# Kernel optimization log

Hardware: AMD Instinct MI355X
Metric: run time of the kernel (lower is better)

The kernel has to match this reference:

```python
import jax, jax.numpy as jnp
import numpy as np

NUM_HEADS = 8


def setup_inputs() -> dict:
    key = jax.random.key(0)
    ks = jax.random.split(key, 6)
    B, E, L = 8, 256, 4096
    top_k = 256
    return {
        "query": jax.random.normal(ks[0], (B, E, L), jnp.float32),
        "keys": jax.random.normal(ks[1], (B, E, L), jnp.float32),
        "values": jax.random.normal(ks[2], (B, E, L), jnp.float32),
        "rand_token_ind": jax.random.randint(ks[3], (B, top_k), 0, L),
        "in_proj_weight": jax.random.normal(ks[4], (3 * E, E), jnp.float32) / np.float32(np.sqrt(E)),
        "in_proj_bias": jnp.zeros((3 * E,), jnp.float32),
        "out_proj_weight": jax.random.normal(ks[5], (E, E), jnp.float32) / np.float32(np.sqrt(E)),
        "out_proj_bias": jnp.zeros((E,), jnp.float32),
        "top_k": top_k,
    }


def _forward(query, keys, values, rand_token_ind, in_proj_weight, in_proj_bias,
             out_proj_weight, out_proj_bias, top_k):
    B, E, Lq = query.shape
    # flatten(2).transpose(-1,-2): channel-first -> [B, L, E]
    q = jnp.swapaxes(query, 1, 2)
    k = jnp.swapaxes(keys, 1, 2)
    v = jnp.swapaxes(values, 1, 2)

    # --- dist_to_random_Q_selection ---
    # random subset of queries, [B, S, E]
    Q_small = jnp.take_along_axis(q, rand_token_ind[:, :, None], axis=1)

    # running min over subset queries of L1 distance (avoids [B,Lk,S,D] blowup)
    def step(min_d, qs):  # qs: [B, E]
        d = jnp.sum(jnp.abs(k - qs[:, None, :]), axis=-1)  # [B, Lk]
        return jnp.minimum(min_d, d), None

    init = jnp.full((B, k.shape[1]), jnp.inf, dtype=k.dtype)
    min_d, _ = jax.lax.scan(step, init, jnp.swapaxes(Q_small, 0, 1))

    # top_k smallest distances, sorted ascending (torch largest=False, sorted=True)
    _, idx = jax.lax.top_k(-min_d, top_k)  # idx: [B, top_k]
    sk = jnp.take_along_axis(k, idx[:, :, None], axis=1)  # [B, top_k, E]
    sv = jnp.take_along_axis(v, idx[:, :, None], axis=1)

    # --- standard torch MultiheadAttention (batch_first) ---
    Wq, Wk, Wv = jnp.split(in_proj_weight, 3, axis=0)
    bq, bk, bv = jnp.split(in_proj_bias, 3, axis=0)
    hd = E // NUM_HEADS
    scale = hd ** -0.5

    def heads(x):
        return x.reshape(x.shape[0], x.shape[1], NUM_HEADS, hd)

    qh = heads(q @ Wq.T + bq) * scale      # [B, Lq, H, hd]
    kh = heads(sk @ Wk.T + bk)             # [B, K,  H, hd]
    vh = heads(sv @ Wv.T + bv)

    scores = jnp.einsum('bqhd,bkhd->bhqk', qh, kh)
    attn = jax.nn.softmax(scores, axis=-1)
    o = jnp.einsum('bhqk,bkhd->bqhd', attn, vh).reshape(B, Lq, E)
    out = o @ out_proj_weight.T + out_proj_bias  # [B, Lq, E]

    # transpose back to original [B, E, Lq] layout
    return jnp.swapaxes(out, 1, 2)


def reference(query, keys, values, rand_token_ind, in_proj_weight, in_proj_bias,
              out_proj_weight, out_proj_bias, top_k):
    return _forward(query, keys, values, rand_token_ind, in_proj_weight,
                    in_proj_bias, out_proj_weight, out_proj_bias, top_k)
```

## Files before the change

kernel.cpp:

```cpp
#include <hip/hip_runtime.h>
#include <math.h>

#define B_SZ   8
#define E_DIM  256
#define L_SEQ  4096
#define S_TOP  256
#define NHEAD  8
#define HD     32
#define NSPLIT 4
#define JSPL   8

typedef __attribute__((ext_vector_type(8))) short bf16x8;
typedef __attribute__((ext_vector_type(4))) float f32x4;

__device__ inline short f2bf(float x) {
    union { float f; unsigned u; } v; v.f = x;
    unsigned r = (v.u + 0x7fff + ((v.u >> 16) & 1)) >> 16;
    return (short)r;
}
__device__ inline float bf2f(short h) {
    union { unsigned u; float f; } c; c.u = ((unsigned)(unsigned short)h) << 16;
    return c.f;
}

__global__ __launch_bounds__(256) void k_gather(const float* __restrict__ query,
                                                const int* __restrict__ ind,
                                                float* __restrict__ qs_pack) {
    int t = blockIdx.x * 256 + threadIdx.x;
    int e = t & (E_DIM - 1);
    int s = (t >> 8) & (S_TOP - 1);
    int b = t >> 16;
    int idx = ind[b * S_TOP + s];
    qs_pack[t] = query[((size_t)b * E_DIM + e) * L_SEQ + idx];
}

__global__ __launch_bounds__(256) void k_dist(const float* __restrict__ keys,
                                              const float* __restrict__ qs_pack,
                                              double* __restrict__ minpart) {
    const int b  = blockIdx.z;
    const int ss = blockIdx.y;
    const int l0 = blockIdx.x * 64;
    const int lid = threadIdx.x;
    const int tx = lid & 15;
    const int ty = lid >> 4;
    __shared__ float Ks[32][64];
    __shared__ float Qs[64][36];
    double (*red)[64] = (double(*)[64])&Ks[0][0];

    const float* kb = keys + (size_t)b * E_DIM * L_SEQ + l0;
    const float* qb = qs_pack + ((size_t)b * S_TOP + ss * 64) * E_DIM;

    double d[4][4];
#pragma unroll
    for (int i = 0; i < 4; ++i)
#pragma unroll
        for (int j = 0; j < 4; ++j) d[i][j] = 0.0;

    for (int c0 = 0; c0 < E_DIM; c0 += 32) {
        __syncthreads();
#pragma unroll
        for (int r = 0; r < 2; ++r) {
            int f4 = lid + 256 * r;
            int e  = f4 >> 4, l4 = (f4 & 15) * 4;
            *(float4*)&Ks[e][l4] = *(const float4*)(kb + (size_t)(c0 + e) * L_SEQ + l4);
            int s  = f4 >> 3, e4 = (f4 & 7) * 4;
            *(float4*)&Qs[s][e4] = *(const float4*)(qb + (size_t)s * E_DIM + c0 + e4);
        }
        __syncthreads();

        float cs[4][4] = {};
#pragma unroll
        for (int e4 = 0; e4 < 32; e4 += 4) {
            float qv[4][4];
#pragma unroll
            for (int j = 0; j < 4; ++j) {
                float4 q = *(const float4*)&Qs[ty * 4 + j][e4];
                qv[j][0] = q.x; qv[j][1] = q.y; qv[j][2] = q.z; qv[j][3] = q.w;
            }
#pragma unroll
            for (int ee = 0; ee < 4; ++ee) {
                float kv[4];
#pragma unroll
                for (int i = 0; i < 4; ++i) kv[i] = Ks[e4 + ee][tx * 4 + i];
#pragma unroll
                for (int i = 0; i < 4; ++i)
#pragma unroll
                    for (int j = 0; j < 4; ++j)
                        cs[i][j] += fabsf(kv[i] - qv[j][ee]);
            }
        }
#pragma unroll
        for (int i = 0; i < 4; ++i)
#pragma unroll
            for (int j = 0; j < 4; ++j) d[i][j] += (double)cs[i][j];
    }

    double md[4];
#pragma unroll
    for (int i = 0; i < 4; ++i) {
        double m = d[i][0];
        m = fmin(m, d[i][1]);
        m = fmin(m, d[i][2]);
        m = fmin(m, d[i][3]);
        md[i] = m;
    }
    __syncthreads();
#pragma unroll
    for (int i = 0; i < 4; ++i) red[ty][tx * 4 + i] = md[i];
    __syncthreads();
    if (lid < 64) {
        double m = red[0][lid];
#pragma unroll
        for (int t = 1; t < 16; ++t) m = fmin(m, red[t][lid]);
        minpart[((size_t)(b * NSPLIT + ss)) * L_SEQ + l0 + lid] = m;
    }
}

__global__ __launch_bounds__(256) void k_rankpart(const double* __restrict__ minpart,
                                                  int* __restrict__ rankpart) {
    const int b  = blockIdx.z;
    const int js = blockIdx.y;
    const int l  = blockIdx.x * 256 + threadIdx.x;
    __shared__ double sd[512];
    const double* mp = minpart + (size_t)b * NSPLIT * L_SEQ;
    for (int jj = threadIdx.x; jj < 512; jj += 256) {
        const int j = js * 512 + jj;
        double v = mp[j];
        v = fmin(v, mp[L_SEQ + j]);
        v = fmin(v, mp[2 * L_SEQ + j]);
        v = fmin(v, mp[3 * L_SEQ + j]);
        sd[jj] = v;
    }
    double dl = mp[l];
    dl = fmin(dl, mp[L_SEQ + l]);
    dl = fmin(dl, mp[2 * L_SEQ + l]);
    dl = fmin(dl, mp[3 * L_SEQ + l]);
    __syncthreads();
    const int jbase = js * 512;
    int rank = 0;
#pragma unroll 8
    for (int jj = 0; jj < 512; ++jj) {
        double dj = sd[jj];
        rank += (dj < dl) || (dj == dl && (jbase + jj) < l) ? 1 : 0;
    }
    rankpart[((size_t)(b * JSPL + js)) * L_SEQ + l] = rank;
}

__global__ __launch_bounds__(256) void k_sel(const int* __restrict__ rankpart,
                                             int* __restrict__ sel) {
    const int t = blockIdx.x * 256 + threadIdx.x;
    const int b = t >> 12;
    const int l = t & (L_SEQ - 1);
    int r = 0;
#pragma unroll
    for (int s = 0; s < JSPL; ++s)
        r += rankpart[((size_t)(b * JSPL + s)) * L_SEQ + l];
    if (r < S_TOP) sel[b * S_TOP + r] = l;
}

__global__ __launch_bounds__(256) void k_kvproj2(const float* __restrict__ keys,
                                                 const float* __restrict__ vals,
                                                 const int* __restrict__ sel,
                                                 const float* __restrict__ Wk,
                                                 const float* __restrict__ bk,
                                                 const float* __restrict__ Wv,
                                                 const float* __restrict__ bv,
                                                 short* __restrict__ khb,
                                                 short* __restrict__ vtb) {
    const int b  = blockIdx.z;
    const int f0 = blockIdx.x * 64;
    const int TR = blockIdx.y >> 2;
    const int k0 = (blockIdx.y & 3) * 64;
    const float* src  = TR ? vals : keys;
    const float* W    = TR ? Wv : Wk;
    const float* bias = TR ? bv : bk;
    const int tx = threadIdx.x, ty = threadIdx.y;
    const int lid = ty * 16 + tx;
    __shared__ float As[16][68];
    __shared__ float Ws[16][68];
    float c[4][4] = {};
    const float* sb = src + (size_t)b * E_DIM * L_SEQ;
    const int* selb = sel + b * S_TOP;
    for (int e0 = 0; e0 < E_DIM; e0 += 16) {
        {
            int e  = lid >> 4;
            int k4 = (lid & 15) * 4;
#pragma unroll
            for (int c2 = 0; c2 < 4; ++c2) {
                int kk = k4 + c2;
                As[e][kk] = sb[(size_t)(e0 + e) * L_SEQ + selb[k0 + kk]];
            }
        }
        {
            int f  = lid >> 2;
            int e4 = (lid & 3) * 4;
            float4 w = *(const float4*)(W + (size_t)(f0 + f) * E_DIM + e0 + e4);
            Ws[e4 + 0][f] = w.x; Ws[e4 + 1][f] = w.y;
            Ws[e4 + 2][f] = w.z; Ws[e4 + 3][f] = w.w;
        }
        __syncthreads();
#pragma unroll
        for (int e = 0; e < 16; ++e) {
            float4 a = *(const float4*)&As[e][ty * 4];
            float4 w = *(const float4*)&Ws[e][tx * 4];
            float av[4] = {a.x, a.y, a.z, a.w};
            float wv[4] = {w.x, w.y, w.z, w.w};
#pragma unroll
            for (int i = 0; i < 4; ++i)
#pragma unroll
                for (int j = 0; j < 4; ++j) c[i][j] += av[i] * wv[j];
        }
        __syncthreads();
    }
    if (TR == 0) {
#pragma unroll
        for (int i = 0; i < 4; ++i) {
            short4 o;
            o.x = f2bf(c[i][0] + bias[f0 + tx * 4 + 0]);
            o.y = f2bf(c[i][1] + bias[f0 + tx * 4 + 1]);
            o.z = f2bf(c[i][2] + bias[f0 + tx * 4 + 2]);
            o.w = f2bf(c[i][3] + bias[f0 + tx * 4 + 3]);
            *(short4*)(khb + ((size_t)b * S_TOP + k0 + ty * 4 + i) * E_DIM + f0 + tx * 4) = o;
        }
    } else {
#pragma unroll
        for (int j = 0; j < 4; ++j) {
            const float bvv = bias[f0 + tx * 4 + j];
            short4 o;
            o.x = f2bf(c[0][j] + bvv); o.y = f2bf(c[1][j] + bvv);
            o.z = f2bf(c[2][j] + bvv); o.w = f2bf(c[3][j] + bvv);
            *(short4*)(vtb + ((size_t)b * E_DIM + f0 + tx * 4 + j) * S_TOP + k0 + ty * 4) = o;
        }
    }
}

__global__ __launch_bounds__(256) void k_wconv(const float* __restrict__ wq,
                                               const float* __restrict__ wo,
                                               short* __restrict__ wqhi,
                                               short* __restrict__ wqlo,
                                               short* __restrict__ wohi,
                                               short* __restrict__ wolo) {
    int t = blockIdx.x * 256 + threadIdx.x;
    float xq = wq[t];
    short hq = f2bf(xq);
    wqhi[t] = hq;
    wqlo[t] = f2bf(xq - bf2f(hq));
    float xo = wo[t];
    short ho = f2bf(xo);
    wohi[t] = ho;
    wolo[t] = f2bf(xo - bf2f(ho));
}

__global__ __launch_bounds__(256) void k_qconv(const float* __restrict__ query,
                                               short* __restrict__ qhi,
                                               short* __restrict__ qlo) {
    const int b  = blockIdx.z;
    const int e0 = blockIdx.y * 64;
    const int l0 = blockIdx.x * 64;
    __shared__ float T[64][68];
    const float* src = query + ((size_t)b * E_DIM + e0) * L_SEQ + l0;
#pragma unroll
    for (int r = 0; r < 4; ++r) {
        int idx = threadIdx.x + 256 * r;
        int e = idx >> 4, l4 = (idx & 15) * 4;
        *(float4*)&T[e][l4] = *(const float4*)(src + (size_t)e * L_SEQ + l4);
    }
    __syncthreads();
    const int l  = threadIdx.x >> 2;
    const int ec = (threadIdx.x & 3) * 16;
    size_t dst = ((size_t)b * L_SEQ + l0 + l) * E_DIM + e0 + ec;
    bf16x8 h0, h1, lo0, lo1;
#pragma unroll
    for (int k = 0; k < 8; ++k) {
        float x = T[ec + k][l];
        short h = f2bf(x);
        h0[k] = h; lo0[k] = f2bf(x - bf2f(h));
    }
#pragma unroll
    for (int k = 0; k < 8; ++k) {
        float x = T[ec + 8 + k][l];
        short h = f2bf(x);
        h1[k] = h; lo1[k] = f2bf(x - bf2f(h));
    }
    *(bf16x8*)(qhi + dst)     = h0;
    *(bf16x8*)(qhi + dst + 8) = h1;
    *(bf16x8*)(qlo + dst)     = lo0;
    *(bf16x8*)(qlo + dst + 8) = lo1;
}

__global__ __launch_bounds__(256) void k_qgemm(const short* __restrict__ qhi,
                                               const short* __restrict__ qlo,
                                               const short* __restrict__ wqhi,
                                               const short* __restrict__ wqlo,
                                               const float* __restrict__ bias,
                                               short* __restrict__ qhb,
                                               float scale) {
    const int b  = blockIdx.z;
    const int f0 = blockIdx.x * 128;
    const int l0 = blockIdx.y * 128;
    const int lid  = threadIdx.x;
    const int wv   = lid >> 6;
    const int lane = lid & 63;
    const int quad = lane >> 4;
    const int m    = lane & 15;
    const int wf   = wv >> 1;
    const int wl   = wv & 1;

    __shared__ short Awh[128 * 40];
    __shared__ short Awl[128 * 40];
    __shared__ short Bqh[128 * 40];
    __shared__ short Bql[128 * 40];

    const short* wh_g = wqhi + (size_t)f0 * E_DIM;
    const short* wl_g = wqlo + (size_t)f0 * E_DIM;
    const short* qh_g = qhi + ((size_t)b * L_SEQ + l0) * E_DIM;
    const short* ql_g = qlo + ((size_t)b * L_SEQ + l0) * E_DIM;

    f32x4 acc[4][4];
    const f32x4 zero = {0.f, 0.f, 0.f, 0.f};
#pragma unroll
    for (int i = 0; i < 4; ++i)
#pragma unroll
        for (int j = 0; j < 4; ++j) acc[i][j] = zero;

    for (int k0 = 0; k0 < E_DIM; k0 += 32) {
        __syncthreads();
#pragma unroll
        for (int r = 0; r < 2; ++r) {
            int idx = lid + 256 * r;
            int row = idx >> 2;
            int kc  = (idx & 3) * 8;
            *(bf16x8*)&Awh[row * 40 + kc] = *(const bf16x8*)(wh_g + (size_t)row * E_DIM + k0 + kc);
            *(bf16x8*)&Awl[row * 40 + kc] = *(const bf16x8*)(wl_g + (size_t)row * E_DIM + k0 + kc);
            *(bf16x8*)&Bqh[row * 40 + kc] = *(const bf16x8*)(qh_g + (size_t)row * E_DIM + k0 + kc);
            *(bf16x8*)&Bql[row * 40 + kc] = *(const bf16x8*)(ql_g + (size_t)row * E_DIM + k0 + kc);
        }
        __syncthreads();

        bf16x8 ah[4], al[4], bh[4], bl[4];
#pragma unroll
        for (int tf = 0; tf < 4; ++tf) {
            int row = wf * 64 + tf * 16 + m;
            ah[tf] = *(const bf16x8*)&Awh[row * 40 + quad * 8];
            al[tf] = *(const bf16x8*)&Awl[row * 40 + quad * 8];
        }
#pragma unroll
        for (int tl = 0; tl < 4; ++tl) {
            int row = wl * 64 + tl * 16 + m;
            bh[tl] = *(const bf16x8*)&Bqh[row * 40 + quad * 8];
            bl[tl] = *(const bf16x8*)&Bql[row * 40 + quad * 8];
        }
#pragma unroll
        for (int tf = 0; tf < 4; ++tf)
#pragma unroll
            for (int tl = 0; tl < 4; ++tl) {
                acc[tf][tl] = __builtin_amdgcn_mfma_f32_16x16x32_bf16(al[tf], bh[tl], acc[tf][tl], 0, 0, 0);
                acc[tf][tl] = __builtin_amdgcn_mfma_f32_16x16x32_bf16(ah[tf], bl[tl], acc[tf][tl], 0, 0, 0);
                acc[tf][tl] = __builtin_amdgcn_mfma_f32_16x16x32_bf16(ah[tf], bh[tl], acc[tf][tl], 0, 0, 0);
            }
    }

#pragma unroll
    for (int tf = 0; tf < 4; ++tf) {
        const int fb = f0 + wf * 64 + tf * 16 + quad * 4;
        float bv0 = bias[fb + 0], bv1 = bias[fb + 1];
        float bv2 = bias[fb + 2], bv3 = bias[fb + 3];
#pragma unroll
        for (int tl = 0; tl < 4; ++tl) {
            const int l = l0 + wl * 64 + tl * 16 + m;
            short4 o;
            o.x = f2bf(scale * (acc[tf][tl][0] + bv0));
            o.y = f2bf(scale * (acc[tf][tl][1] + bv1));
            o.z = f2bf(scale * (acc[tf][tl][2] + bv2));
            o.w = f2bf(scale * (acc[tf][tl][3] + bv3));
            *(short4*)(qhb + ((size_t)b * L_SEQ + l) * E_DIM + fb) = o;
        }
    }
}

__global__ __launch_bounds__(256) void k_attn(const short* __restrict__ qhb,
                                              const short* __restrict__ khb,
                                              const short* __restrict__ vtb,
                                              short* __restrict__ ohi,
                                              short* __restrict__ olo) {
    __shared__ short P[4][16][264];
    const int b = blockIdx.z, h = blockIdx.y;
    const int wv   = threadIdx.x >> 6;
    const int lane = threadIdx.x & 63;
    const int quad = lane >> 4;
    const int m    = lane & 15;
    const int l0 = blockIdx.x * 64 + wv * 16;

    const short* qp = qhb + ((size_t)b * L_SEQ + l0 + m) * E_DIM + h * HD + quad * 8;
    const bf16x8 qa = *(const bf16x8*)qp;

    const short* kb = khb + (size_t)b * S_TOP * E_DIM + h * HD + quad * 8;
    f32x4 sacc[16];
    const f32x4 zero = {0.f, 0.f, 0.f, 0.f};
#pragma unroll
    for (int t = 0; t < 16; ++t) {
        bf16x8 kf = *(const bf16x8*)(kb + (size_t)(t * 16 + m) * E_DIM);
        sacc[t] = __builtin_amdgcn_mfma_f32_16x16x32_bf16(qa, kf, zero, 0, 0, 0);
    }

    float mx[4], ssum[4];
#pragma unroll
    for (int r = 0; r < 4; ++r) {
        float v = sacc[0][r];
#pragma unroll
        for (int t = 1; t < 16; ++t) v = fmaxf(v, sacc[t][r]);
#pragma unroll
        for (int off = 1; off < 16; off <<= 1) v = fmaxf(v, __shfl_xor(v, off, 16));
        mx[r] = v;
        ssum[r] = 0.f;
    }
#pragma unroll
    for (int t = 0; t < 16; ++t) {
#pragma unroll
        for (int r = 0; r < 4; ++r) {
            float p = __expf(sacc[t][r] - mx[r]);
            ssum[r] += p;
            P[wv][quad * 4 + r][t * 16 + m] = f2bf(p);
        }
    }
#pragma unroll
    for (int r = 0; r < 4; ++r) {
        float v = ssum[r];
#pragma unroll
        for (int off = 1; off < 16; off <<= 1) v += __shfl_xor(v, off, 16);
        ssum[r] = v;
    }

    const short* vb = vtb + ((size_t)b * E_DIM + h * HD) * S_TOP;
    f32x4 oacc[2];
#pragma unroll
    for (int dt = 0; dt < 2; ++dt) {
        f32x4 acc = zero;
#pragma unroll
        for (int k0 = 0; k0 < S_TOP; k0 += 32) {
            bf16x8 pa = *(const bf16x8*)&P[wv][m][k0 + quad * 8];
            bf16x8 vf = *(const bf16x8*)(vb + (size_t)(dt * 16 + m) * S_TOP + k0 + quad * 8);
            acc = __builtin_amdgcn_mfma_f32_16x16x32_bf16(pa, vf, acc, 0, 0, 0);
        }
        oacc[dt] = acc;
    }

    short* oph = ohi + ((size_t)b * L_SEQ + l0) * E_DIM + h * HD;
    short* opl = olo + ((size_t)b * L_SEQ + l0) * E_DIM + h * HD;
#pragma unroll
    for (int r = 0; r < 4; ++r) {
        const float inv = 1.0f / ssum[r];
#pragma unroll
        for (int dt = 0; dt < 2; ++dt) {
            float val = oacc[dt][r] * inv;
            short hh = f2bf(val);
            size_t off = (size_t)(quad * 4 + r) * E_DIM + dt * 16 + m;
            oph[off] = hh;
            opl[off] = f2bf(val - bf2f(hh));
        }
    }
}

__global__ __launch_bounds__(256) void k_ogemm(const short* __restrict__ ohi,
                                               const short* __restrict__ olo,
                                               const short* __restrict__ wohi,
                                               const short* __restrict__ wolo,
                                               const float* __restrict__ bias,
                                               float* __restrict__ out) {
    const int b  = blockIdx.z;
    const int f0 = blockIdx.x * 128;
    const int l0 = blockIdx.y * 128;
    const int lid  = threadIdx.x;
    const int wv   = lid >> 6;
    const int lane = lid & 63;
    const int quad = lane >> 4;
    const int m    = lane & 15;
    const int wl   = wv >> 1;
    const int wf   = wv & 1;

    __shared__ short Aoh[128 * 40];
    __shared__ short Aol[128 * 40];
    __shared__ short Bwh[128 * 40];
    __shared__ short Bwl[128 * 40];

    const short* oh_g = ohi + ((size_t)b * L_SEQ + l0) * E_DIM;
    const short* ol_g = olo + ((size_t)b * L_SEQ + l0) * E_DIM;
    const short* wh_g = wohi + (size_t)f0 * E_DIM;
    const short* wl_g = wolo + (size_t)f0 * E_DIM;

    f32x4 acc[4][4];
    const f32x4 zero = {0.f, 0.f, 0.f, 0.f};
#pragma unroll
    for (int i = 0; i < 4; ++i)
#pragma unroll
        for (int j = 0; j < 4; ++j) acc[i][j] = zero;

    for (int k0 = 0; k0 < E_DIM; k0 += 32) {
        __syncthreads();
#pragma unroll
        for (int r = 0; r < 2; ++r) {
            int idx = lid + 256 * r;
            int row = idx >> 2;
            int kc  = (idx & 3) * 8;
            *(bf16x8*)&Aoh[row * 40 + kc] = *(const bf16x8*)(oh_g + (size_t)row * E_DIM + k0 + kc);
            *(bf16x8*)&Aol[row * 40 + kc] = *(const bf16x8*)(ol_g + (size_t)row * E_DIM + k0 + kc);
            *(bf16x8*)&Bwh[row * 40 + kc] = *(const bf16x8*)(wh_g + (size_t)row * E_DIM + k0 + kc);
            *(bf16x8*)&Bwl[row * 40 + kc] = *(const bf16x8*)(wl_g + (size_t)row * E_DIM + k0 + kc);
        }
        __syncthreads();

        bf16x8 ah[4], al[4], bh[4], bl[4];
#pragma unroll
        for (int tl = 0; tl < 4; ++tl) {
            int row = wl * 64 + tl * 16 + m;
            ah[tl] = *(const bf16x8*)&Aoh[row * 40 + quad * 8];
            al[tl] = *(const bf16x8*)&Aol[row * 40 + quad * 8];
        }
#pragma unroll
        for (int tf = 0; tf < 4; ++tf) {
            int row = wf * 64 + tf * 16 + m;
            bh[tf] = *(const bf16x8*)&Bwh[row * 40 + quad * 8];
            bl[tf] = *(const bf16x8*)&Bwl[row * 40 + quad * 8];
        }
#pragma unroll
        for (int tl = 0; tl < 4; ++tl)
#pragma unroll
            for (int tf = 0; tf < 4; ++tf) {
                acc[tl][tf] = __builtin_amdgcn_mfma_f32_16x16x32_bf16(al[tl], bh[tf], acc[tl][tf], 0, 0, 0);
                acc[tl][tf] = __builtin_amdgcn_mfma_f32_16x16x32_bf16(ah[tl], bl[tf], acc[tl][tf], 0, 0, 0);
                acc[tl][tf] = __builtin_amdgcn_mfma_f32_16x16x32_bf16(ah[tl], bh[tf], acc[tl][tf], 0, 0, 0);
            }
    }

#pragma unroll
    for (int tl = 0; tl < 4; ++tl) {
        const int lb = l0 + wl * 64 + tl * 16 + quad * 4;
#pragma unroll
        for (int tf = 0; tf < 4; ++tf) {
            const int f = f0 + wf * 64 + tf * 16 + m;
            const float bv = bias[f];
            float4 o;
            o.x = acc[tl][tf][0] + bv;
            o.y = acc[tl][tf][1] + bv;
            o.z = acc[tl][tf][2] + bv;
            o.w = acc[tl][tf][3] + bv;
            *(float4*)(out + ((size_t)b * E_DIM + f) * L_SEQ + lb) = o;
        }
    }
}

extern "C" void kernel_launch(void* const* d_in, const int* in_sizes, int n_in,
                              void* d_out, int out_size, void* d_ws, size_t ws_size,
                              hipStream_t stream) {
    const float* query = (const float*)d_in[0];
    const float* keys  = (const float*)d_in[1];
    const float* vals  = (const float*)d_in[2];
    const int*   rind  = (const int*)d_in[3];
    const float* ipw   = (const float*)d_in[4];
    const float* ipb   = (const float*)d_in[5];
    const float* opw   = (const float*)d_in[6];
    const float* opb   = (const float*)d_in[7];
    float* out = (float*)d_out;

    char* ws = (char*)d_ws;
    const size_t MI = 1024 * 1024;
    float*  qs_pack  = (float*)(ws + 0);
    double* minpart  = (double*)(ws + 2 * MI);
    int*    sel      = (int*)   (ws + 3 * MI);
    short*  khb      = (short*) (ws + 4 * MI);
    int*    rankpart = (int*)   (ws + 5 * MI);
    short*  vtb      = (short*) (ws + 6 * MI);
    short*  wqhi     = (short*) (ws + 7 * MI);
    short*  wqlo     = (short*) (ws + 7 * MI + 131072);
    short*  wohi     = (short*) (ws + 7 * MI + 2 * 131072);
    short*  wolo     = (short*) (ws + 7 * MI + 3 * 131072);
    short*  qhb      = (short*) (ws + 8 * MI);
    short*  qhi      = (short*) (ws + 24 * MI);
    short*  qlo      = (short*) (ws + 40 * MI);
    short*  ohi      = (short*) (ws + 24 * MI);
    short*  olo      = (short*) (ws + 40 * MI);

    const float scale = 0.17677669529663687f;

    k_gather<<<dim3((B_SZ * E_DIM * S_TOP) / 256), 256, 0, stream>>>(query, rind, qs_pack);
    k_dist<<<dim3(L_SEQ / 64, NSPLIT, B_SZ), dim3(256), 0, stream>>>(keys, qs_pack, minpart);
    k_rankpart<<<dim3(L_SEQ / 256, JSPL, B_SZ), 256, 0, stream>>>(minpart, rankpart);
    k_sel<<<dim3((B_SZ * L_SEQ) / 256), 256, 0, stream>>>(rankpart, sel);
    k_kvproj2<<<dim3(E_DIM / 64, 2 * (S_TOP / 64), B_SZ), dim3(16, 16), 0, stream>>>(
        keys, vals, sel,
        ipw + (size_t)E_DIM * E_DIM, ipb + E_DIM,
        ipw + (size_t)2 * E_DIM * E_DIM, ipb + 2 * E_DIM,
        khb, vtb);
    k_wconv<<<dim3(256), 256, 0, stream>>>(ipw, opw, wqhi, wqlo, wohi, wolo);
    k_qconv<<<dim3(L_SEQ / 64, E_DIM / 64, B_SZ), 256, 0, stream>>>(query, qhi, qlo);
    k_qgemm<<<dim3(E_DIM / 128, L_SEQ / 128, B_SZ), 256, 0, stream>>>(
        qhi, qlo, wqhi, wqlo, ipb, qhb, scale);
    k_attn<<<dim3(L_SEQ / 64, NHEAD, B_SZ), 256, 0, stream>>>(qhb, khb, vtb, ohi, olo);
    k_ogemm<<<dim3(E_DIM / 128, L_SEQ / 128, B_SZ), 256, 0, stream>>>(
        ohi, olo, wohi, wolo, opb, out);
}
```

Before: 440.0 us.

## Merge gather, weight and query conversion into one prep kernel; prefetch k_dist tiles

Three independent preprocessing kernels (query subset gather, weight hi/lo bf16 split, query transpose/split) are merged into a single launch that dispatches on block index, cutting two kernel launches and letting the work run concurrently. Separately, k_dist now register-prefetches the next K/Q chunk from global memory while computing the current one, to hide load latency. The prep fusion adds shared-memory allocation to the gather and weight blocks, and the prefetch raises register pressure in a kernel already holding double accumulators.

```diff
diff --git a/kernel.cpp b/kernel.cpp
--- a/kernel.cpp
+++ b/kernel.cpp
@@ -23,15 +23,72 @@
     return c.f;
 }
 
-__global__ __launch_bounds__(256) void k_gather(const float* __restrict__ query,
-                                                const int* __restrict__ ind,
-                                                float* __restrict__ qs_pack) {
-    int t = blockIdx.x * 256 + threadIdx.x;
-    int e = t & (E_DIM - 1);
-    int s = (t >> 8) & (S_TOP - 1);
-    int b = t >> 16;
-    int idx = ind[b * S_TOP + s];
-    qs_pack[t] = query[((size_t)b * E_DIM + e) * L_SEQ + idx];
+__global__ __launch_bounds__(256) void k_prep(const float* __restrict__ query,
+                                              const int* __restrict__ ind,
+                                              const float* __restrict__ wq,
+                                              const float* __restrict__ wo,
+                                              float* __restrict__ qs_pack,
+                                              short* __restrict__ wqhi,
+                                              short* __restrict__ wqlo,
+                                              short* __restrict__ wohi,
+                                              short* __restrict__ wolo,
+                                              short* __restrict__ qhi,
+                                              short* __restrict__ qlo) {
+    __shared__ float T[64][68];
+    const int blk = blockIdx.x;
+    if (blk < 2048) {
+        int t = blk * 256 + threadIdx.x;
+        int e = t & (E_DIM - 1);
+        int s = (t >> 8) & (S_TOP - 1);
+        int b = t >> 16;
+        int idx = ind[b * S_TOP + s];
+        qs_pack[t] = query[((size_t)b * E_DIM + e) * L_SEQ + idx];
+        return;
+    }
+    if (blk >= 4096) {
+        int t = (blk - 4096) * 256 + threadIdx.x;
+        float xq = wq[t];
+        short hq = f2bf(xq);
+        wqhi[t] = hq;
+        wqlo[t] = f2bf(xq - bf2f(hq));
+        float xo = wo[t];
+        short ho = f2bf(xo);
+        wohi[t] = ho;
+        wolo[t] = f2bf(xo - bf2f(ho));
+        return;
+    }
+    const int idx = blk - 2048;
+    const int b  = idx >> 8;
+    const int e0 = ((idx >> 6) & 3) * 64;
+    const int l0 = (idx & 63) * 64;
+    const float* src = query + ((size_t)b * E_DIM + e0) * L_SEQ + l0;
+#pragma unroll
+    for (int r = 0; r < 4; ++r) {
+        int i2 = threadIdx.x + 256 * r;
+        int e = i2 >> 4, l4 = (i2 & 15) * 4;
+        *(float4*)&T[e][l4] = *(const float4*)(src + (size_t)e * L_SEQ + l4);
+    }
+    __syncthreads();
+    const int l  = threadIdx.x >> 2;
+    const int ec = (threadIdx.x & 3) * 16;
+    size_t dst = ((size_t)b * L_SEQ + l0 + l) * E_DIM + e0 + ec;
+    bf16x8 h0, h1, lo0, lo1;
+#pragma unroll
+    for (int k = 0; k < 8; ++k) {
+        float x = T[ec + k][l];
+        short h = f2bf(x);
+        h0[k] = h; lo0[k] = f2bf(x - bf2f(h));
+    }
+#pragma unroll
+    for (int k = 0; k < 8; ++k) {
+        float x = T[ec + 8 + k][l];
+        short h = f2bf(x);
+        h1[k] = h; lo1[k] = f2bf(x - bf2f(h));
+    }
+    *(bf16x8*)(qhi + dst)     = h0;
+    *(bf16x8*)(qhi + dst + 8) = h1;
+    *(bf16x8*)(qlo + dst)     = lo0;
+    *(bf16x8*)(qlo + dst + 8) = lo1;
 }
 
 __global__ __launch_bounds__(256) void k_dist(const float* __restrict__ keys,
@@ -56,17 +113,40 @@
 #pragma unroll
         for (int j = 0; j < 4; ++j) d[i][j] = 0.0;
 
-    for (int c0 = 0; c0 < E_DIM; c0 += 32) {
-        __syncthreads();
+    float4 pk[2], pq[2];
+    {
 #pragma unroll
         for (int r = 0; r < 2; ++r) {
             int f4 = lid + 256 * r;
             int e  = f4 >> 4, l4 = (f4 & 15) * 4;
-            *(float4*)&Ks[e][l4] = *(const float4*)(kb + (size_t)(c0 + e) * L_SEQ + l4);
+            pk[r] = *(const float4*)(kb + (size_t)e * L_SEQ + l4);
             int s  = f4 >> 3, e4 = (f4 & 7) * 4;
-            *(float4*)&Qs[s][e4] = *(const float4*)(qb + (size_t)s * E_DIM + c0 + e4);
-        }
-        __syncthreads();
+            pq[r] = *(const float4*)(qb + (size_t)s * E_DIM + e4);
+        }
+    }
+
+    for (int c0 = 0; c0 < E_DIM; c0 += 32) {
+        __syncthreads();
+#pragma unroll
+        for (int r = 0; r < 2; ++r) {
+            int f4 = lid + 256 * r;
+            int e  = f4 >> 4, l4 = (f4 & 15) * 4;
+            *(float4*)&Ks[e][l4] = pk[r];
+            int s  = f4 >> 3, e4 = (f4 & 7) * 4;
+            *(float4*)&Qs[s][e4] = pq[r];
+        }
+        __syncthreads();
+        if (c0 + 32 < E_DIM) {
+            const int cn = c0 + 32;
+#pragma unroll
+            for (int r = 0; r < 2; ++r) {
+                int f4 = lid + 256 * r;
+                int e  = f4 >> 4, l4 = (f4 & 15) * 4;
+                pk[r] = *(const float4*)(kb + (size_t)(cn + e) * L_SEQ + l4);
+                int s  = f4 >> 3, e4 = (f4 & 7) * 4;
+                pq[r] = *(const float4*)(qb + (size_t)s * E_DIM + cn + e4);
+            }
+        }
 
         float cs[4][4] = {};
 #pragma unroll
@@ -234,60 +314,6 @@
     }
 }
 
-__global__ __launch_bounds__(256) void k_wconv(const float* __restrict__ wq,
-                                               const float* __restrict__ wo,
-                                               short* __restrict__ wqhi,
-                                               short* __restrict__ wqlo,
-                                               short* __restrict__ wohi,
-                                               short* __restrict__ wolo) {
-    int t = blockIdx.x * 256 + threadIdx.x;
-    float xq = wq[t];
-    short hq = f2bf(xq);
-    wqhi[t] = hq;
-    wqlo[t] = f2bf(xq - bf2f(hq));
-    float xo = wo[t];
-    short ho = f2bf(xo);
-    wohi[t] = ho;
-    wolo[t] = f2bf(xo - bf2f(ho));
-}
-
-__global__ __launch_bounds__(256) void k_qconv(const float* __restrict__ query,
-                                               short* __restrict__ qhi,
-                                               short* __restrict__ qlo) {
-    const int b  = blockIdx.z;
-    const int e0 = blockIdx.y * 64;
-    const int l0 = blockIdx.x * 64;
-    __shared__ float T[64][68];
-    const float* src = query + ((size_t)b * E_DIM + e0) * L_SEQ + l0;
-#pragma unroll
-    for (int r = 0; r < 4; ++r) {
-        int idx = threadIdx.x + 256 * r;
-        int e = idx >> 4, l4 = (idx & 15) * 4;
-        *(float4*)&T[e][l4] = *(const float4*)(src + (size_t)e * L_SEQ + l4);
-    }
-    __syncthreads();
-    const int l  = threadIdx.x >> 2;
-    const int ec = (threadIdx.x & 3) * 16;
-    size_t dst = ((size_t)b * L_SEQ + l0 + l) * E_DIM + e0 + ec;
-    bf16x8 h0, h1, lo0, lo1;
-#pragma unroll
-    for (int k = 0; k < 8; ++k) {
-        float x = T[ec + k][l];
-        short h = f2bf(x);
-        h0[k] = h; lo0[k] = f2bf(x - bf2f(h));
-    }
-#pragma unroll
-    for (int k = 0; k < 8; ++k) {
-        float x = T[ec + 8 + k][l];
-        short h = f2bf(x);
-        h1[k] = h; lo1[k] = f2bf(x - bf2f(h));
-    }
-    *(bf16x8*)(qhi + dst)     = h0;
-    *(bf16x8*)(qhi + dst + 8) = h1;
-    *(bf16x8*)(qlo + dst)     = lo0;
-    *(bf16x8*)(qlo + dst + 8) = lo1;
-}
-
 __global__ __launch_bounds__(256) void k_qgemm(const short* __restrict__ qhi,
                                                const short* __restrict__ qlo,
                                                const short* __restrict__ wqhi,
@@ -582,7 +608,8 @@
 
     const float scale = 0.17677669529663687f;
 
-    k_gather<<<dim3((B_SZ * E_DIM * S_TOP) / 256), 256, 0, stream>>>(query, rind, qs_pack);
+    k_prep<<<dim3(4352), 256, 0, stream>>>(query, rind, ipw, opw, qs_pack,
+                                           wqhi, wqlo, wohi, wolo, qhi, qlo);
     k_dist<<<dim3(L_SEQ / 64, NSPLIT, B_SZ), dim3(256), 0, stream>>>(keys, qs_pack, minpart);
     k_rankpart<<<dim3(L_SEQ / 256, JSPL, B_SZ), 256, 0, stream>>>(minpart, rankpart);
     k_sel<<<dim3((B_SZ * L_SEQ) / 256), 256, 0, stream>>>(rankpart, sel);
@@ -591,8 +618,6 @@
         ipw + (size_t)E_DIM * E_DIM, ipb + E_DIM,
         ipw + (size_t)2 * E_DIM * E_DIM, ipb + 2 * E_DIM,
         khb, vtb);
-    k_wconv<<<dim3(256), 256, 0, stream>>>(ipw, opw, wqhi, wqlo, wohi, wolo);
-    k_qconv<<<dim3(L_SEQ / 64, E_DIM / 64, B_SZ), 256, 0, stream>>>(query, qhi, qlo);
     k_qgemm<<<dim3(E_DIM / 128, L_SEQ / 128, B_SZ), 256, 0, stream>>>(
         qhi, qlo, wqhi, wqlo, ipb, qhb, scale);
     k_attn<<<dim3(L_SEQ / 64, NHEAD, B_SZ), 256, 0, stream>>>(qhb, khb, vtb, ohi, olo);
```

New measurement: 470.3 us. 1.07x slower.
